# Kernel optimization log

Measured on AMD Instinct MI355X. Metric: run time of the kernel, lower is better.

The kernel has to match this reference:

```python
import jax, jax.numpy as jnp
import numpy as np

D = 4096
H = 4 * D
EPS = 1e-5


def layer_norm(x, g, b):
    mu = jnp.mean(x, axis=-1, keepdims=True)
    var = jnp.mean(jnp.square(x - mu), axis=-1, keepdims=True)
    return (x - mu) * jax.lax.rsqrt(var + EPS) * g + b


def setup_inputs() -> dict:
    key = jax.random.key(0)
    ks = jax.random.split(key, 8)
    s = 0.02
    return {
        "x": jax.random.normal(ks[0], (2, 2048, D), dtype=jnp.float32),
        "Wq": jax.random.normal(ks[1], (D, D), dtype=jnp.float32) * s,
        "bq": jnp.zeros((D,), jnp.float32),
        "Wk": jax.random.normal(ks[2], (D, D), dtype=jnp.float32) * s,
        "bk": jnp.zeros((D,), jnp.float32),
        "Wv": jax.random.normal(ks[3], (D, D), dtype=jnp.float32) * s,
        "bv": jnp.zeros((D,), jnp.float32),
        "Wo": jax.random.normal(ks[4], (D, D), dtype=jnp.float32) * s,
        "bo": jnp.zeros((D,), jnp.float32),
        "g1": jnp.ones((D,), jnp.float32),
        "b1": jnp.zeros((D,), jnp.float32),
        "g2": jnp.ones((D,), jnp.float32),
        "b2": jnp.zeros((D,), jnp.float32),
        "W1": jax.random.normal(ks[5], (D, H), dtype=jnp.float32) * s,
        "bi1": jnp.zeros((H,), jnp.float32),
        "W2": jax.random.normal(ks[6], (H, D), dtype=jnp.float32) * s,
        "bi2": jnp.zeros((D,), jnp.float32),
    }


def reference(x, Wq, bq, Wk, bk, Wv, bv, Wo, bo, g1, b1, g2, b2, W1, bi1, W2, bi2):
    # single-head attention, scale = sqrt(D) (as in the source)
    Q = x @ Wq + bq          # [B, S, D]
    K = x @ Wk + bk
    V = x @ Wv + bv
    scores = jnp.einsum("bsd,btd->bst", Q, K) / jnp.sqrt(jnp.float32(D))
    attn = jax.nn.softmax(scores, axis=-1) @ V   # [B, S, D]
    x = attn @ Wo + bo + x
    x = layer_norm(x, g1, b1)
    h = jax.nn.gelu(x @ W1 + bi1, approximate=False)  # torch nn.GELU default = exact erf
    x = h @ W2 + bi2 + x
    x = layer_norm(x, g2, b2)
    return x
```

## Files before the change

kernel.cpp:

```cpp
#include <hip/hip_runtime.h>
#include <hip/hip_bf16.h>

typedef __bf16 bf16x8 __attribute__((ext_vector_type(8)));
typedef float  f32x4  __attribute__((ext_vector_type(4)));
typedef unsigned short u16;
typedef unsigned int   u32;

#define DEV __device__ __forceinline__

DEV float bu2f(u16 u){ union{u32 i; float f;} x; x.i=((u32)u)<<16; return x.f; }
DEV u16 f2bu(float f){ union{float f; u32 i;} x; x.f=f; u32 r=x.i+0x7FFFu+((x.i>>16)&1u); return (u16)(r>>16); }
DEV u32 pack2(float a, float b){ return (u32)f2bu(a) | ((u32)f2bu(b)<<16); }

DEV void gload16(const void* g, void* l){
  __builtin_amdgcn_global_load_lds((const __attribute__((address_space(1))) void*)g,
                                   (__attribute__((address_space(3))) void*)l, 16, 0, 0);
}

template<int BIAS, int GELU, int RESF32, int OUTF32>
__global__ __launch_bounds__(256) void gemm_bt(
    const u16* __restrict__ A, const u16* __restrict__ Bt,
    const float* __restrict__ bias, const float* __restrict__ resid,
    float* __restrict__ outF, u16* __restrict__ outB,
    int M, int N, int K,
    long long sA, long long sB, long long sC)
{
  __shared__ __align__(16) u16 As[128*64];
  __shared__ __align__(16) u16 Bs[128*64];
  const int tid  = threadIdx.x;
  const int lane = tid & 63;
  const int wave = tid >> 6;
  const int wm = wave >> 1, wn = wave & 1;
  const int rowBase = blockIdx.y * 128;
  const int colBase = blockIdx.x * 128;
  const long long z = blockIdx.z;

  const u16* Ag = A + z*sA + (size_t)rowBase * K;
  const u16* Bg = Bt + z*sB + (size_t)colBase * K;

  const int srow = lane >> 3;
  const int scol = ((lane & 7) ^ srow) * 8;
  const int q   = lane >> 4;
  const int s7  = lane & 7;
  const int r15 = lane & 15;

  f32x4 acc[4][4];
  const f32x4 fzero = {0.f,0.f,0.f,0.f};
#pragma unroll
  for (int m=0;m<4;++m)
#pragma unroll
    for (int n=0;n<4;++n) acc[m][n]=fzero;

  for (int kt=0; kt<K; kt+=64){
#pragma unroll
    for (int i=0;i<4;++i){
      const int c = wave*4 + i;
      gload16(Ag + (size_t)(c*8+srow)*K + kt + scol, (void*)(As + c*512 + lane*8));
      gload16(Bg + (size_t)(c*8+srow)*K + kt + scol, (void*)(Bs + c*512 + lane*8));
    }
    __syncthreads();
#pragma unroll
    for (int h=0; h<2; ++h){
      bf16x8 av[4], bv4[4];
#pragma unroll
      for (int m=0;m<4;++m)
        av[m]  = *reinterpret_cast<const bf16x8*>(&As[(wm*64+m*16+r15)*64 + (((h*4+q)^s7)*8)]);
#pragma unroll
      for (int n=0;n<4;++n)
        bv4[n] = *reinterpret_cast<const bf16x8*>(&Bs[(wn*64+n*16+r15)*64 + (((h*4+q)^s7)*8)]);
#pragma unroll
      for (int m=0;m<4;++m)
#pragma unroll
        for (int n=0;n<4;++n)
          acc[m][n] = __builtin_amdgcn_mfma_f32_16x16x32_bf16(av[m], bv4[n], acc[m][n], 0,0,0);
    }
    __syncthreads();
  }

  const long long cb = z*sC;
#pragma unroll
  for (int m=0;m<4;++m){
    const int row0 = rowBase + wm*64 + m*16 + q*4;
#pragma unroll
    for (int n=0;n<4;++n){
      const int col = colBase + wn*64 + n*16 + r15;
      float bb = 0.f;
      if (BIAS) bb = bias[col];
#pragma unroll
      for (int r=0;r<4;++r){
        float v = acc[m][n][r] + bb;
        if (GELU) v = 0.5f*v*(1.f+erff(v*0.70710678118654752f));
        const size_t oi = (size_t)cb + (size_t)(row0+r)*N + col;
        if (RESF32) v += resid[oi];
        if (OUTF32) outF[oi] = v;
        else        outB[oi] = f2bu(v);
      }
    }
  }
}

__global__ __launch_bounds__(256) void tr_f32_bf16(
    const float* __restrict__ in, u16* __restrict__ out, int R, int C)
{
  __shared__ float tile[64][65];
  const int t = threadIdx.x;
  const int tr = blockIdx.y*64, tc = blockIdx.x*64;
  const int c4 = (t&15)*4;
#pragma unroll
  for (int i=0;i<4;++i){
    const int r = i*16 + (t>>4);
    const float4 v = *reinterpret_cast<const float4*>(&in[(size_t)(tr+r)*C + tc + c4]);
    tile[r][c4+0]=v.x; tile[r][c4+1]=v.y; tile[r][c4+2]=v.z; tile[r][c4+3]=v.w;
  }
  __syncthreads();
#pragma unroll
  for (int i=0;i<4;++i){
    const int c = i*16 + (t>>4);
    uint2 o;
    o.x = pack2(tile[c4+0][c], tile[c4+1][c]);
    o.y = pack2(tile[c4+2][c], tile[c4+3][c]);
    *reinterpret_cast<uint2*>(&out[(size_t)(tc+c)*R + tr + c4]) = o;
  }
}

__global__ __launch_bounds__(256) void tr_bf16(
    const u16* __restrict__ in, u16* __restrict__ out, int R, int C,
    long long sIn, long long sOut)
{
  __shared__ u16 tile[64][72];
  const long long z = blockIdx.z;
  in  += z*sIn; out += z*sOut;
  const int t = threadIdx.x;
  const int tr = blockIdx.y*64, tc = blockIdx.x*64;
  const int c4 = (t&15)*4;
#pragma unroll
  for (int i=0;i<4;++i){
    const int r = i*16 + (t>>4);
    const uint2 v = *reinterpret_cast<const uint2*>(&in[(size_t)(tr+r)*C + tc + c4]);
    tile[r][c4+0]=(u16)(v.x&0xffffu); tile[r][c4+1]=(u16)(v.x>>16);
    tile[r][c4+2]=(u16)(v.y&0xffffu); tile[r][c4+3]=(u16)(v.y>>16);
  }
  __syncthreads();
#pragma unroll
  for (int i=0;i<4;++i){
    const int c = i*16 + (t>>4);
    uint2 o;
    o.x = (u32)tile[c4+0][c] | ((u32)tile[c4+1][c]<<16);
    o.y = (u32)tile[c4+2][c] | ((u32)tile[c4+3][c]<<16);
    *reinterpret_cast<uint2*>(&out[(size_t)(tc+c)*R + tr + c4]) = o;
  }
}

__global__ __launch_bounds__(256) void cvt_f32_bf16(
    const float* __restrict__ in, u16* __restrict__ out, int n4)
{
  const int i = blockIdx.x*256 + threadIdx.x;
  if (i >= n4) return;
  const float4 v = reinterpret_cast<const float4*>(in)[i];
  uint2 o; o.x = pack2(v.x,v.y); o.y = pack2(v.z,v.w);
  reinterpret_cast<uint2*>(out)[i] = o;
}

__global__ __launch_bounds__(256) void softmax2048(
    const float* __restrict__ S, u16* __restrict__ P, float scale)
{
  const size_t row = blockIdx.x;
  const float4* src = reinterpret_cast<const float4*>(S + row*2048);
  const int t = threadIdx.x, lane = t&63, wave = t>>6;
  const float4 a = src[t], b = src[t+256];
  float v[8] = {a.x,a.y,a.z,a.w,b.x,b.y,b.z,b.w};
  float m = -3.4e38f;
#pragma unroll
  for (int i=0;i<8;++i){ v[i]*=scale; m = fmaxf(m, v[i]); }
#pragma unroll
  for (int o=32;o>0;o>>=1) m = fmaxf(m, __shfl_xor(m, o));
  __shared__ float red[8];
  if (lane==0) red[wave]=m;
  __syncthreads();
  m = fmaxf(fmaxf(red[0],red[1]), fmaxf(red[2],red[3]));
  float s = 0.f;
#pragma unroll
  for (int i=0;i<8;++i){ v[i] = __expf(v[i]-m); s += v[i]; }
#pragma unroll
  for (int o=32;o>0;o>>=1) s += __shfl_xor(s, o);
  if (lane==0) red[4+wave]=s;
  __syncthreads();
  s = red[4]+red[5]+red[6]+red[7];
  const float r = 1.f/s;
  uint2 o1, o2;
  o1.x = pack2(v[0]*r, v[1]*r); o1.y = pack2(v[2]*r, v[3]*r);
  o2.x = pack2(v[4]*r, v[5]*r); o2.y = pack2(v[6]*r, v[7]*r);
  uint2* dst = reinterpret_cast<uint2*>(P + row*2048);
  dst[t] = o1; dst[t+256] = o2;
}

template<int WB>
__global__ __launch_bounds__(256) void layernorm4096(
    const float* __restrict__ X, const float* __restrict__ g,
    const float* __restrict__ b, float* __restrict__ Yf, u16* __restrict__ Yb)
{
  const size_t row = blockIdx.x;
  const float4* src = reinterpret_cast<const float4*>(X + row*4096);
  const int t = threadIdx.x, lane = t&63, wave = t>>6;
  float4 xv[4];
  float sum=0.f, ss=0.f;
#pragma unroll
  for (int i=0;i<4;++i){
    xv[i] = src[t + 256*i];
    sum += xv[i].x+xv[i].y+xv[i].z+xv[i].w;
    ss  += xv[i].x*xv[i].x + xv[i].y*xv[i].y + xv[i].z*xv[i].z + xv[i].w*xv[i].w;
  }
#pragma unroll
  for (int o=32;o>0;o>>=1){ sum += __shfl_xor(sum,o); ss += __shfl_xor(ss,o); }
  __shared__ float rs[4], rq[4];
  if (lane==0){ rs[wave]=sum; rq[wave]=ss; }
  __syncthreads();
  sum = rs[0]+rs[1]+rs[2]+rs[3];
  ss  = rq[0]+rq[1]+rq[2]+rq[3];
  const float mean = sum * (1.f/4096.f);
  const float var  = ss * (1.f/4096.f) - mean*mean;
  const float rstd = rsqrtf(var + 1e-5f);
#pragma unroll
  for (int i=0;i<4;++i){
    const int i4 = t + 256*i;
    const float4 gv = reinterpret_cast<const float4*>(g)[i4];
    const float4 bvv = reinterpret_cast<const float4*>(b)[i4];
    float4 y;
    y.x = (xv[i].x-mean)*rstd*gv.x + bvv.x;
    y.y = (xv[i].y-mean)*rstd*gv.y + bvv.y;
    y.z = (xv[i].z-mean)*rstd*gv.z + bvv.z;
    y.w = (xv[i].w-mean)*rstd*gv.w + bvv.w;
    reinterpret_cast<float4*>(Yf + row*4096)[i4] = y;
    if (WB){
      uint2 o; o.x = pack2(y.x,y.y); o.y = pack2(y.z,y.w);
      reinterpret_cast<uint2*>(Yb + row*4096)[i4] = o;
    }
  }
}

extern "C" void kernel_launch(void* const* d_in, const int* in_sizes, int n_in,
                              void* d_out, int out_size, void* d_ws, size_t ws_size,
                              hipStream_t stream)
{
  constexpr int D = 4096, HD = 16384, S = 2048, B = 2;
  constexpr int NT = B*S;
  const float* x   = (const float*)d_in[0];
  const float* Wq  = (const float*)d_in[1];
  const float* bq  = (const float*)d_in[2];
  const float* Wk  = (const float*)d_in[3];
  const float* bk  = (const float*)d_in[4];
  const float* Wv  = (const float*)d_in[5];
  const float* bvp = (const float*)d_in[6];
  const float* Wo  = (const float*)d_in[7];
  const float* bo  = (const float*)d_in[8];
  const float* g1  = (const float*)d_in[9];
  const float* b1  = (const float*)d_in[10];
  const float* g2  = (const float*)d_in[11];
  const float* b2  = (const float*)d_in[12];
  const float* W1  = (const float*)d_in[13];
  const float* bi1 = (const float*)d_in[14];
  const float* W2  = (const float*)d_in[15];
  const float* bi2 = (const float*)d_in[16];

  char* ws = (char*)d_ws;
  const size_t MB32 = 33554432;
  u16* WqT = (u16*)(ws + 0*MB32);
  u16* WkT = (u16*)(ws + 1*MB32);
  u16* WvT = (u16*)(ws + 2*MB32);
  u16* WoT = (u16*)(ws + 3*MB32);
  u16* W1T = (u16*)(ws + 0*MB32);
  u16* xb  = (u16*)(ws + 4*MB32);
  u16* Qb  = (u16*)(ws + 5*MB32);
  u16* Kb  = (u16*)(ws + 6*MB32);
  u16* Vb  = (u16*)(ws + 7*MB32);
  u16* W2T = (u16*)(ws + 4*MB32);
  u16* Vt  = (u16*)(ws + 8*MB32);
  float* scoresF = (float*)(ws + 9*MB32);
  u16* Pb  = (u16*)(ws + 10*MB32);
  u16* Ab  = (u16*)(ws + 10*MB32 + 16777216);
  u16* hB  = (u16*)(ws + 8*MB32);
  float* x1raw = (float*)(ws + 12*MB32);
  float* x2raw = (float*)(ws + 12*MB32);
  float* x1f   = (float*)(ws + 14*MB32);
  u16*   x1b   = (u16*)(ws + 16*MB32);

  const dim3 blk(256);
  const long long SD = (long long)S*D, SS = (long long)S*S, DS = (long long)D*S;

  tr_f32_bf16<<<dim3(D/64, D/64), blk, 0, stream>>>(Wq, WqT, D, D);
  tr_f32_bf16<<<dim3(D/64, D/64), blk, 0, stream>>>(Wk, WkT, D, D);
  tr_f32_bf16<<<dim3(D/64, D/64), blk, 0, stream>>>(Wv, WvT, D, D);
  tr_f32_bf16<<<dim3(D/64, D/64), blk, 0, stream>>>(Wo, WoT, D, D);
  cvt_f32_bf16<<<dim3((NT*D/4)/256), blk, 0, stream>>>(x, xb, NT*D/4);

  gemm_bt<1,0,0,0><<<dim3(D/128, NT/128, 1), blk, 0, stream>>>(xb, WqT, bq,  nullptr, nullptr, Qb, NT, D, D, 0,0,0);
  gemm_bt<1,0,0,0><<<dim3(D/128, NT/128, 1), blk, 0, stream>>>(xb, WkT, bk,  nullptr, nullptr, Kb, NT, D, D, 0,0,0);
  gemm_bt<1,0,0,0><<<dim3(D/128, NT/128, 1), blk, 0, stream>>>(xb, WvT, bvp, nullptr, nullptr, Vb, NT, D, D, 0,0,0);
  tr_bf16<<<dim3(D/64, S/64, B), blk, 0, stream>>>(Vb, Vt, S, D, SD, SD);

  gemm_bt<0,0,0,1><<<dim3(S/128, S/128, B), blk, 0, stream>>>(Qb, Kb, nullptr, nullptr, scoresF, nullptr, S, S, D, SD, SD, SS);
  softmax2048<<<dim3(B*S), blk, 0, stream>>>(scoresF, Pb, 0.015625f);
  gemm_bt<0,0,0,0><<<dim3(D/128, S/128, B), blk, 0, stream>>>(Pb, Vt, nullptr, nullptr, nullptr, Ab, S, D, S, SS, DS, SD);

  gemm_bt<1,0,1,1><<<dim3(D/128, NT/128, 1), blk, 0, stream>>>(Ab, WoT, bo, x, x1raw, nullptr, NT, D, D, 0,0,0);
  layernorm4096<1><<<dim3(NT), blk, 0, stream>>>(x1raw, g1, b1, x1f, x1b);

  tr_f32_bf16<<<dim3(HD/64, D/64), blk, 0, stream>>>(W1, W1T, D, HD);
  gemm_bt<1,1,0,0><<<dim3(HD/128, NT/128, 1), blk, 0, stream>>>(x1b, W1T, bi1, nullptr, nullptr, hB, NT, HD, D, 0,0,0);
  tr_f32_bf16<<<dim3(D/64, HD/64), blk, 0, stream>>>(W2, W2T, HD, D);
  gemm_bt<1,0,1,1><<<dim3(D/128, NT/128, 1), blk, 0, stream>>>(hB, W2T, bi2, x1f, x2raw, nullptr, NT, D, HD, 0,0,0);
  layernorm4096<0><<<dim3(NT), blk, 0, stream>>>(x2raw, g2, b2, (float*)d_out, nullptr);
}
```

Measured before the change: 2.612 ms.

## Replace 128x128 GEMM with 256x256 multi-buffered pipelined GEMM and XCD swizzle

The GEMM kernel becomes a 256x256 tile with 512 threads and 8 waves, each wave computing a 128x64 sub-tile. It streams K in 32-wide slices through a 4-deep LDS ring buffer, keeping three slices in flight with explicit vmcnt waits and one barrier per step, and raises wave priority around the MFMA block. An optional block-index swizzle groups work across the 8 XCDs for better L2 reuse. Larger tiles cut global traffic per FLOP and the prefetch hides load latency, but this costs 128 KB of LDS and many accumulator registers, which limits occupancy.

```diff
diff --git a/kernel.cpp b/kernel.cpp
--- a/kernel.cpp
+++ b/kernel.cpp
@@ -8,79 +8,110 @@
 
 #define DEV __device__ __forceinline__
 
-DEV float bu2f(u16 u){ union{u32 i; float f;} x; x.i=((u32)u)<<16; return x.f; }
 DEV u16 f2bu(float f){ union{float f; u32 i;} x; x.f=f; u32 r=x.i+0x7FFFu+((x.i>>16)&1u); return (u16)(r>>16); }
 DEV u32 pack2(float a, float b){ return (u32)f2bu(a) | ((u32)f2bu(b)<<16); }
 
-DEV void gload16(const void* g, void* l){
+DEV void gload16(const u16* g, u16* l){
   __builtin_amdgcn_global_load_lds((const __attribute__((address_space(1))) void*)g,
                                    (__attribute__((address_space(3))) void*)l, 16, 0, 0);
 }
 
 template<int BIAS, int GELU, int RESF32, int OUTF32>
-__global__ __launch_bounds__(256) void gemm_bt(
+__global__ __launch_bounds__(512, 2) void gemm256(
     const u16* __restrict__ A, const u16* __restrict__ Bt,
     const float* __restrict__ bias, const float* __restrict__ resid,
     float* __restrict__ outF, u16* __restrict__ outB,
-    int M, int N, int K,
+    int M, int N, int K, int SWZ,
     long long sA, long long sB, long long sC)
 {
-  __shared__ __align__(16) u16 As[128*64];
-  __shared__ __align__(16) u16 Bs[128*64];
+  __shared__ __align__(16) u16 As[4][8192];
+  __shared__ __align__(16) u16 Bs[4][8192];
+
   const int tid  = threadIdx.x;
   const int lane = tid & 63;
   const int wave = tid >> 6;
-  const int wm = wave >> 1, wn = wave & 1;
-  const int rowBase = blockIdx.y * 128;
-  const int colBase = blockIdx.x * 128;
-  const long long z = blockIdx.z;
-
-  const u16* Ag = A + z*sA + (size_t)rowBase * K;
-  const u16* Bg = Bt + z*sB + (size_t)colBase * K;
-
-  const int srow = lane >> 3;
-  const int scol = ((lane & 7) ^ srow) * 8;
-  const int q   = lane >> 4;
-  const int s7  = lane & 7;
+  const int wm = wave >> 2;
+  const int wn = wave & 3;
+
+  int bx = blockIdx.x, by = blockIdx.y;
+  if (SWZ) {
+    const int gx = gridDim.x;
+    const int nwg = gx * gridDim.y;
+    const int flat = by * gx + bx;
+    const int cpx = nwg >> 3;
+    const int s = (flat & 7) * cpx + (flat >> 3);
+    bx = s % gx; by = s / gx;
+  }
+  const int rowBase = by * 256;
+  const int colBase = bx * 256;
+
+  const u16* Ag = A + (size_t)blockIdx.z * sA + (size_t)rowBase * K;
+  const u16* Bg = Bt + (size_t)blockIdx.z * sB + (size_t)colBase * K;
+
+  const int qsw = (lane & 3) ^ ((lane >> 3) & 3);
+  const u16* apA0 = Ag + (size_t)(wave*32 + (lane>>2)) * K + qsw*8;
+  const u16* apA1 = apA0 + (size_t)16 * K;
+  const u16* apB0 = Bg + (size_t)(wave*32 + (lane>>2)) * K + qsw*8;
+  const u16* apB1 = apB0 + (size_t)16 * K;
+  u16* dA0 = &As[0][wave*1024 + lane*8];
+  u16* dA1 = dA0 + 512;
+  u16* dB0 = &Bs[0][wave*1024 + lane*8];
+  u16* dB1 = dB0 + 512;
+
+#define STAGE(t) { const int _b = (t) & 3; const size_t _k = (size_t)(t) * 32;          \
+    gload16(apA0 + _k, dA0 + _b*8192); gload16(apA1 + _k, dA1 + _b*8192);               \
+    gload16(apB0 + _k, dB0 + _b*8192); gload16(apB1 + _k, dB1 + _b*8192); }
+
   const int r15 = lane & 15;
-
-  f32x4 acc[4][4];
-  const f32x4 fzero = {0.f,0.f,0.f,0.f};
-#pragma unroll
-  for (int m=0;m<4;++m)
-#pragma unroll
-    for (int n=0;n<4;++n) acc[m][n]=fzero;
-
-  for (int kt=0; kt<K; kt+=64){
-#pragma unroll
-    for (int i=0;i<4;++i){
-      const int c = wave*4 + i;
-      gload16(Ag + (size_t)(c*8+srow)*K + kt + scol, (void*)(As + c*512 + lane*8));
-      gload16(Bg + (size_t)(c*8+srow)*K + kt + scol, (void*)(Bs + c*512 + lane*8));
-    }
-    __syncthreads();
-#pragma unroll
-    for (int h=0; h<2; ++h){
-      bf16x8 av[4], bv4[4];
-#pragma unroll
-      for (int m=0;m<4;++m)
-        av[m]  = *reinterpret_cast<const bf16x8*>(&As[(wm*64+m*16+r15)*64 + (((h*4+q)^s7)*8)]);
+  const int gp  = (lane >> 4) ^ ((lane >> 1) & 3);
+  const u16* rdA = &As[0][(wm*128 + r15)*32 + gp*8];
+  const u16* rdB = &Bs[0][(wn*64  + r15)*32 + gp*8];
+
+  f32x4 acc[8][4];
+  const f32x4 fz = {0.f,0.f,0.f,0.f};
+#pragma unroll
+  for (int m=0;m<8;++m)
+#pragma unroll
+    for (int n=0;n<4;++n) acc[m][n] = fz;
+
+  const int KT = K >> 5;
+  STAGE(0);
+  if (KT > 1) STAGE(1);
+  if (KT > 2) STAGE(2);
+
+  for (int t = 0; t < KT; ++t) {
+    const int rem = KT - t;
+    if (rem > 2)      asm volatile("s_waitcnt vmcnt(8)" ::: "memory");
+    else if (rem > 1) asm volatile("s_waitcnt vmcnt(4)" ::: "memory");
+    else              asm volatile("s_waitcnt vmcnt(0)" ::: "memory");
+    __builtin_amdgcn_s_barrier();
+    asm volatile("" ::: "memory");
+
+    const u16* pa = rdA + (t & 3) * 8192;
+    const u16* pb = rdB + (t & 3) * 8192;
+    bf16x8 a[8], b[4];
+#pragma unroll
+    for (int m=0;m<8;++m) a[m] = *(const bf16x8*)(pa + m*512);
+#pragma unroll
+    for (int n=0;n<4;++n) b[n] = *(const bf16x8*)(pb + n*512);
+
+    if (t + 3 < KT) STAGE(t + 3);
+
+    __builtin_amdgcn_s_setprio(1);
+#pragma unroll
+    for (int m=0;m<8;++m)
 #pragma unroll
       for (int n=0;n<4;++n)
-        bv4[n] = *reinterpret_cast<const bf16x8*>(&Bs[(wn*64+n*16+r15)*64 + (((h*4+q)^s7)*8)]);
-#pragma unroll
-      for (int m=0;m<4;++m)
-#pragma unroll
-        for (int n=0;n<4;++n)
-          acc[m][n] = __builtin_amdgcn_mfma_f32_16x16x32_bf16(av[m], bv4[n], acc[m][n], 0,0,0);
-    }
-    __syncthreads();
-  }
-
-  const long long cb = z*sC;
-#pragma unroll
-  for (int m=0;m<4;++m){
-    const int row0 = rowBase + wm*64 + m*16 + q*4;
+        acc[m][n] = __builtin_amdgcn_mfma_f32_16x16x32_bf16(a[m], b[n], acc[m][n], 0,0,0);
+    __builtin_amdgcn_s_setprio(0);
+  }
+#undef STAGE
+
+  const long long cb = (long long)blockIdx.z * sC;
+  const int q4 = (lane >> 4) * 4;
+#pragma unroll
+  for (int m=0;m<8;++m){
+    const int row0 = rowBase + wm*128 + m*16 + q4;
 #pragma unroll
     for (int n=0;n<4;++n){
       const int col = colBase + wn*64 + n*16 + r15;
@@ -284,7 +315,7 @@
   float* x1f   = (float*)(ws + 14*MB32);
   u16*   x1b   = (u16*)(ws + 16*MB32);
 
-  const dim3 blk(256);
+  const dim3 blk(256), blkG(512);
   const long long SD = (long long)S*D, SS = (long long)S*S, DS = (long long)D*S;
 
   tr_f32_bf16<<<dim3(D/64, D/64), blk, 0, stream>>>(Wq, WqT, D, D);
@@ -293,21 +324,21 @@
   tr_f32_bf16<<<dim3(D/64, D/64), blk, 0, stream>>>(Wo, WoT, D, D);
   cvt_f32_bf16<<<dim3((NT*D/4)/256), blk, 0, stream>>>(x, xb, NT*D/4);
 
-  gemm_bt<1,0,0,0><<<dim3(D/128, NT/128, 1), blk, 0, stream>>>(xb, WqT, bq,  nullptr, nullptr, Qb, NT, D, D, 0,0,0);
-  gemm_bt<1,0,0,0><<<dim3(D/128, NT/128, 1), blk, 0, stream>>>(xb, WkT, bk,  nullptr, nullptr, Kb, NT, D, D, 0,0,0);
-  gemm_bt<1,0,0,0><<<dim3(D/128, NT/128, 1), blk, 0, stream>>>(xb, WvT, bvp, nullptr, nullptr, Vb, NT, D, D, 0,0,0);
+  gemm256<1,0,0,0><<<dim3(D/256, NT/256, 1), blkG, 0, stream>>>(xb, WqT, bq,  nullptr, nullptr, Qb, NT, D, D, 1, 0,0,0);
+  gemm256<1,0,0,0><<<dim3(D/256, NT/256, 1), blkG, 0, stream>>>(xb, WkT, bk,  nullptr, nullptr, Kb, NT, D, D, 1, 0,0,0);
+  gemm256<1,0,0,0><<<dim3(D/256, NT/256, 1), blkG, 0, stream>>>(xb, WvT, bvp, nullptr, nullptr, Vb, NT, D, D, 1, 0,0,0);
   tr_bf16<<<dim3(D/64, S/64, B), blk, 0, stream>>>(Vb, Vt, S, D, SD, SD);
 
-  gemm_bt<0,0,0,1><<<dim3(S/128, S/128, B), blk, 0, stream>>>(Qb, Kb, nullptr, nullptr, scoresF, nullptr, S, S, D, SD, SD, SS);
+  gemm256<0,0,0,1><<<dim3(S/256, S/256, B), blkG, 0, stream>>>(Qb, Kb, nullptr, nullptr, scoresF, nullptr, S, S, D, 0, SD, SD, SS);
   softmax2048<<<dim3(B*S), blk, 0, stream>>>(scoresF, Pb, 0.015625f);
-  gemm_bt<0,0,0,0><<<dim3(D/128, S/128, B), blk, 0, stream>>>(Pb, Vt, nullptr, nullptr, nullptr, Ab, S, D, S, SS, DS, SD);
-
-  gemm_bt<1,0,1,1><<<dim3(D/128, NT/128, 1), blk, 0, stream>>>(Ab, WoT, bo, x, x1raw, nullptr, NT, D, D, 0,0,0);
+  gemm256<0,0,0,0><<<dim3(D/256, S/256, B), blkG, 0, stream>>>(Pb, Vt, nullptr, nullptr, nullptr, Ab, S, D, S, 0, SS, DS, SD);
+
+  gemm256<1,0,1,1><<<dim3(D/256, NT/256, 1), blkG, 0, stream>>>(Ab, WoT, bo, x, x1raw, nullptr, NT, D, D, 1, 0,0,0);
   layernorm4096<1><<<dim3(NT), blk, 0, stream>>>(x1raw, g1, b1, x1f, x1b);
 
   tr_f32_bf16<<<dim3(HD/64, D/64), blk, 0, stream>>>(W1, W1T, D, HD);
-  gemm_bt<1,1,0,0><<<dim3(HD/128, NT/128, 1), blk, 0, stream>>>(x1b, W1T, bi1, nullptr, nullptr, hB, NT, HD, D, 0,0,0);
+  gemm256<1,1,0,0><<<dim3(HD/256, NT/256, 1), blkG, 0, stream>>>(x1b, W1T, bi1, nullptr, nullptr, hB, NT, HD, D, 1, 0,0,0);
   tr_f32_bf16<<<dim3(D/64, HD/64), blk, 0, stream>>>(W2, W2T, HD, D);
-  gemm_bt<1,0,1,1><<<dim3(D/128, NT/128, 1), blk, 0, stream>>>(hB, W2T, bi2, x1f, x2raw, nullptr, NT, D, HD, 0,0,0);
+  gemm256<1,0,1,1><<<dim3(D/256, NT/256, 1), blkG, 0, stream>>>(hB, W2T, bi2, x1f, x2raw, nullptr, NT, D, HD, 1, 0,0,0);
   layernorm4096<0><<<dim3(NT), blk, 0, stream>>>(x2raw, g2, b2, (float*)d_out, nullptr);
 }
```

Result: faster. 2.165 ms (-17.1%).
